# Kernel tuning notes

Hardware: AMD Instinct MI355X
Metric: run time of the kernel (lower is better)

Reference implementation:

```python
import jax, jax.numpy as jnp
import numpy as np

# Gemma-style paged attention, decode-heavy continuous batching
B = 16            # number of sequences in the batch
BLOCK = 64        # KV-cache block size (tokens per block)
MAX_BLOCKS = 32   # max blocks per sequence -> max 2048 KV tokens
NUM_BLOCKS = B * MAX_BLOCKS  # 512 total cache blocks
MAX_KV = MAX_BLOCKS * BLOCK  # 2048
HQ, HK, D = 16, 8, 256       # query heads, kv heads (GQA), head_dim
HIDDEN = 3072
MAX_Q = 4                    # max new (query) tokens per sequence
ROPE_BASE = 10000.0


def setup_inputs() -> dict:
    key = jax.random.key(0)
    ks = jax.random.split(key, 7)
    # deterministic ragged layout
    q_seqlens = np.array([1 + (i % 4) for i in range(B)], np.int64)        # sum = 40
    kv_seqlens = np.array([1024 + (i * 67) % 1025 for i in range(B)], np.int64)
    q_start_loc = np.concatenate([[0], np.cumsum(q_seqlens)[:-1]]).astype(np.int64)
    T = int(q_seqlens.sum())
    history = kv_seqlens - q_seqlens
    position_ids_1d = np.concatenate(
        [np.arange(history[i], kv_seqlens[i]) for i in range(B)]).astype(np.int64)
    block_offsets = np.arange(NUM_BLOCKS, dtype=np.int64).reshape(B, MAX_BLOCKS)
    inv_freq = (1.0 / ROPE_BASE ** (np.arange(0, D, 2) / D)).astype(np.float32)
    return {
        'hidden_states': jax.random.normal(ks[0], (T, HIDDEN), jnp.float32),
        'Wq': jax.random.normal(ks[1], (HIDDEN, HQ * D), jnp.float32) * 0.02,
        'Wk': jax.random.normal(ks[2], (HIDDEN, HK * D), jnp.float32) * 0.02,
        'Wv': jax.random.normal(ks[3], (HIDDEN, HK * D), jnp.float32) * 0.02,
        'Wo': jax.random.normal(ks[4], (HQ * D, HIDDEN), jnp.float32) * 0.02,
        'k_cache': jax.random.normal(ks[5], (NUM_BLOCKS, BLOCK, HK, D), jnp.float32),
        'v_cache': jax.random.normal(ks[6], (NUM_BLOCKS, BLOCK, HK, D), jnp.float32),
        'inv_freq': jnp.asarray(inv_freq),
        'position_ids_1d': jnp.asarray(position_ids_1d),
        'q_start_loc': jnp.asarray(q_start_loc),
        'q_seqlens': jnp.asarray(q_seqlens),
        'kv_seqlens': jnp.asarray(kv_seqlens),
        'block_offsets': jnp.asarray(block_offsets),
    }


def reference(hidden_states, Wq, Wk, Wv, Wo, k_cache, v_cache, inv_freq,
              position_ids_1d, q_start_loc, q_seqlens, kv_seqlens, block_offsets):
    T = hidden_states.shape[0]
    # fused QKV projection
    q = (hidden_states @ Wq).reshape(T, HQ, D)
    k = (hidden_states @ Wk).reshape(T, HK, D)
    v = (hidden_states @ Wv).reshape(T, HK, D)
    # fused rotary embedding (neox / rotate-half style, per-token position ids)
    freqs = position_ids_1d.astype(jnp.float32)[:, None] * inv_freq[None, :]  # [T, D/2]
    cos = jnp.cos(freqs)[:, None, :]
    sin = jnp.sin(freqs)[:, None, :]

    def rope(x):
        x1, x2 = jnp.split(x, 2, axis=-1)
        return jnp.concatenate([x1 * cos - x2 * sin, x2 * cos + x1 * sin], axis=-1)

    q = rope(q)
    k = rope(k)
    # ---- fill_kv_cache: scatter new K/V into paged block cache ----
    tok = jnp.arange(T)
    seq_end = jnp.cumsum(q_seqlens)
    seq_id = jnp.searchsorted(seq_end, tok, side='right')      # sequence of each token
    off = tok - q_start_loc[seq_id]                             # offset within new tokens
    kv_pos = (kv_seqlens - q_seqlens)[seq_id] + off             # absolute kv position
    blk = block_offsets[seq_id, kv_pos // BLOCK]
    slot = kv_pos % BLOCK
    k_cache = k_cache.at[blk, slot].set(k)
    v_cache = v_cache.at[blk, slot].set(v)
    # ---- paged_attention_fwd ----
    # gather each sequence's blocks -> [B, MAX_KV, HK, D]
    k_seq = k_cache[block_offsets].reshape(B, MAX_KV, HK, D)
    v_seq = v_cache[block_offsets].reshape(B, MAX_KV, HK, D)
    # pad queries per sequence -> [B, MAX_Q, HK, G, D]
    qidx = jnp.clip(q_start_loc[:, None] + jnp.arange(MAX_Q)[None, :], 0, T - 1)
    G = HQ // HK
    qpad = q[qidx].reshape(B, MAX_Q, HK, G, D)
    scale = jnp.float32(D) ** -0.5
    scores = jnp.einsum('bqkgd,bskd->bkgqs', qpad * scale, k_seq)  # [B,HK,G,MAX_Q,MAX_KV]
    # causal mask over absolute kv positions (also masks padded kv slots)
    jpos = jnp.arange(MAX_Q)[None, :, None]
    spos = jnp.arange(MAX_KV)[None, None, :]
    mask = spos <= ((kv_seqlens - q_seqlens)[:, None, None] + jpos)  # [B,MAX_Q,MAX_KV]
    scores = jnp.where(mask[:, None, None, :, :], scores, jnp.float32(-1e30))
    attn = jax.nn.softmax(scores, axis=-1)
    out = jnp.einsum('bkgqs,bskd->bqkgd', attn, v_seq).reshape(B, MAX_Q, HQ * D)
    # scatter padded output back to flat token layout
    out_flat = out[seq_id, off]  # [T, HQ*D]
    return out_flat @ Wo
```

## Files before the change

kernel.cpp:

```cpp
#include <hip/hip_runtime.h>
#include <math.h>

#define TT 40
#define NB 16
#define HQn 16
#define HKn 8
#define Gn 2
#define Dn 256
#define HID 3072
#define QKV_COLS 8192
#define NPART 32

#define WAVE_LDS_FENCE() do { \
    asm volatile("s_waitcnt lgkmcnt(0)" ::: "memory"); \
    __builtin_amdgcn_sched_barrier(0); \
  } while (0)

__global__ __launch_bounds__(256) void k1_qkv_gemm(
    const float* __restrict__ hs, const float* __restrict__ Wq,
    const float* __restrict__ Wk, const float* __restrict__ Wv,
    float* __restrict__ part1) {
  const int tile = blockIdx.x & 31;
  const int ks = blockIdx.x >> 5;
  const int c0 = tile << 8;
  const float* W; int ld, cw0;
  if (tile < 16)      { W = Wq; ld = 4096; cw0 = c0; }
  else if (tile < 24) { W = Wk; ld = 2048; cw0 = c0 - 4096; }
  else                { W = Wv; ld = 2048; cw0 = c0 - 6144; }
  const int kbase = ks * 192;
  const int cq = (threadIdx.x & 63) << 2;
  const int r0 = (threadIdx.x >> 6) * 10;
  __shared__ float h_lds[40][64];
  float acc[10][4];
#pragma unroll
  for (int r = 0; r < 10; ++r) { acc[r][0]=0.f; acc[r][1]=0.f; acc[r][2]=0.f; acc[r][3]=0.f; }
  for (int kc = 0; kc < 192; kc += 64) {
    __syncthreads();
    for (int i = threadIdx.x; i < 2560; i += 256) {
      int t = i >> 6, kk = i & 63;
      h_lds[t][kk] = hs[t * HID + kbase + kc + kk];
    }
    __syncthreads();
    const float* wp = W + (size_t)(kbase + kc) * ld + cw0 + cq;
#pragma unroll 2
    for (int k4 = 0; k4 < 16; ++k4) {
      float4 h4[10];
#pragma unroll
      for (int r = 0; r < 10; ++r)
        h4[r] = *reinterpret_cast<const float4*>(&h_lds[r0 + r][k4 << 2]);
#pragma unroll
      for (int j = 0; j < 4; ++j) {
        float4 w4 = *reinterpret_cast<const float4*>(wp + (size_t)((k4 << 2) + j) * ld);
#pragma unroll
        for (int r = 0; r < 10; ++r) {
          float hv = (j == 0) ? h4[r].x : (j == 1) ? h4[r].y
                   : (j == 2) ? h4[r].z : h4[r].w;
          acc[r][0] = fmaf(hv, w4.x, acc[r][0]);
          acc[r][1] = fmaf(hv, w4.y, acc[r][1]);
          acc[r][2] = fmaf(hv, w4.z, acc[r][2]);
          acc[r][3] = fmaf(hv, w4.w, acc[r][3]);
        }
      }
    }
  }
#pragma unroll
  for (int r = 0; r < 10; ++r) {
    int t = r0 + r;
    float4 v = make_float4(acc[r][0], acc[r][1], acc[r][2], acc[r][3]);
    *reinterpret_cast<float4*>(&part1[(size_t)(ks * TT + t) * QKV_COLS + c0 + cq]) = v;
  }
}

__global__ __launch_bounds__(256) void k2_reduce_rope(
    const float* __restrict__ part1, const float* __restrict__ inv_freq,
    const int* __restrict__ pos_ids,
    float* __restrict__ qbuf, float* __restrict__ kbuf, float* __restrict__ vbuf) {
  const int t = blockIdx.x >> 5;
  const int tile = blockIdx.x & 31;
  const int c = (tile << 8) + threadIdx.x;
  float s = 0.f;
#pragma unroll
  for (int ks = 0; ks < 16; ++ks) s += part1[(size_t)(ks * TT + t) * QKV_COLS + c];
  __shared__ float sl[256];
  sl[threadIdx.x] = s;
  __syncthreads();
  if (tile < 24) {
    const int d = threadIdx.x;
    const int d2 = d & 127;
    float fr = (float)pos_ids[t] * inv_freq[d2];
    float cs = cosf(fr), sn = sinf(fr);
    float v = (d < 128) ? (sl[d] * cs - sl[d + 128] * sn)
                        : (sl[d] * cs + sl[d - 128] * sn);
    if (tile < 16) qbuf[t * 4096 + (tile << 8) + d] = v * 0.0625f;
    else           kbuf[t * 2048 + ((tile - 16) << 8) + d] = v;
  } else {
    vbuf[t * 2048 + ((tile - 24) << 8) + threadIdx.x] = s;
  }
}

__global__ __launch_bounds__(256) void k3_attn_partial(
    const float* __restrict__ qbuf, const float* __restrict__ kbuf,
    const float* __restrict__ vbuf, const float* __restrict__ k_cache,
    const float* __restrict__ v_cache, const int* __restrict__ blk_off,
    const int* __restrict__ q_start, const int* __restrict__ q_lens,
    const int* __restrict__ kv_lens,
    float* __restrict__ part_o, float* __restrict__ part_ml) {
  const int seg = blockIdx.x & 7;
  const int hk = (blockIdx.x >> 3) & 7;
  const int b = blockIdx.x >> 6;
  const int kv_len = kv_lens[b];
  if ((seg << 8) >= kv_len) return;
  const int q_cnt = q_lens[b];
  const int hist = kv_len - q_cnt;
  const int q0 = q_start[b];
  const int nq = q_cnt * 2;

  __shared__ float q_lds[8][256];
  __shared__ float S[4][2][64][8];

  const int tid = threadIdx.x;
  const int w = tid >> 6;
  const int lane = tid & 63;

  for (int i = tid; i < 2048; i += 256) {
    int qv = i >> 8, d = i & 255;
    int qtok = min(qv >> 1, q_cnt - 1);
    q_lds[qv][d] = qbuf[(size_t)(q0 + qtok) * 4096 + (hk * Gn + (qv & 1)) * 256 + d];
  }
  __syncthreads();

  const int part = (seg << 2) + w;
  const int sBeg = part << 6;
  if (sBeg >= kv_len) return;

  const int blk = blk_off[(b << 5) + part];
  const float* kb   = k_cache + ((size_t)blk << 17) + ((size_t)hk << 8);
  const float* vb   = v_cache + ((size_t)blk << 17) + ((size_t)hk << 8);
  const float* knew = kbuf + ((size_t)q0 << 11) + ((size_t)hk << 8);
  const float* vnew = vbuf + ((size_t)q0 << 11) + ((size_t)hk << 8);

  const int tp = lane & 7;
  const int qd = lane >> 3;

#pragma unroll
  for (int pass = 0; pass < 2; ++pass) {
    const float* kr[4];
#pragma unroll
    for (int tt = 0; tt < 4; ++tt) {
      int s = sBeg + (pass << 5) + (tp << 2) + tt;
      int sc = s < kv_len ? s : kv_len - 1;
      const float* row = (sc < hist) ? (kb + ((size_t)(sc & 63) << 11))
                                     : (knew + ((size_t)(sc - hist) << 11));
      kr[tt] = row + (qd << 2);
    }
    float acc[4][8];
#pragma unroll
    for (int tt = 0; tt < 4; ++tt)
#pragma unroll
      for (int qv = 0; qv < 8; ++qv) acc[tt][qv] = 0.f;

    float4 kf[2][4];
#pragma unroll
    for (int tt = 0; tt < 4; ++tt)
      kf[0][tt] = *reinterpret_cast<const float4*>(kr[tt]);
#pragma unroll
    for (int c = 0; c < 8; ++c) {
      if (c + 1 < 8) {
#pragma unroll
        for (int tt = 0; tt < 4; ++tt)
          kf[(c + 1) & 1][tt] =
              *reinterpret_cast<const float4*>(kr[tt] + ((c + 1) << 5));
      }
      const float4* kc_ = kf[c & 1];
#pragma unroll
      for (int qv = 0; qv < 8; ++qv) {
        float4 qf = *reinterpret_cast<const float4*>(&q_lds[qv][(qd << 2) + (c << 5)]);
#pragma unroll
        for (int tt = 0; tt < 4; ++tt) {
          acc[tt][qv] = fmaf(qf.x, kc_[tt].x, acc[tt][qv]);
          acc[tt][qv] = fmaf(qf.y, kc_[tt].y, acc[tt][qv]);
          acc[tt][qv] = fmaf(qf.z, kc_[tt].z, acc[tt][qv]);
          acc[tt][qv] = fmaf(qf.w, kc_[tt].w, acc[tt][qv]);
        }
      }
    }
#pragma unroll
    for (int tt = 0; tt < 4; ++tt)
#pragma unroll
      for (int qv = 0; qv < 8; ++qv) {
        float v = acc[tt][qv];
        v += __shfl_xor(v, 8);
        v += __shfl_xor(v, 16);
        acc[tt][qv] = v;
      }
    if ((lane & 24) == 0) {
      const int h = lane >> 5;
#pragma unroll
      for (int tt = 0; tt < 4; ++tt) {
        int srel = (pass << 5) + (tp << 2) + tt;
        *reinterpret_cast<float4*>(&S[w][h][srel][0]) =
            make_float4(acc[tt][0], acc[tt][1], acc[tt][2], acc[tt][3]);
        *reinterpret_cast<float4*>(&S[w][h][srel][4]) =
            make_float4(acc[tt][4], acc[tt][5], acc[tt][6], acc[tt][7]);
      }
    }
  }
  WAVE_LDS_FENCE();

  const int qv2 = lane >> 3;
  const int grp = lane & 7;
  const int pidx8 = (((b * HKn + hk) * NPART + part) << 3);
  float sv[8];
  float mloc = -1e30f;
#pragma unroll
  for (int t = 0; t < 8; ++t) {
    int sl = (t << 3) + grp;
    float v = S[w][0][sl][qv2] + S[w][1][sl][qv2];
    int sAbs = sBeg + sl;
    bool valid = (qv2 < nq) && ((sAbs - hist) <= (qv2 >> 1));
    v = valid ? v : -1e30f;
    sv[t] = v;
    mloc = fmaxf(mloc, v);
  }
  mloc = fmaxf(mloc, __shfl_xor(mloc, 1));
  mloc = fmaxf(mloc, __shfl_xor(mloc, 2));
  mloc = fmaxf(mloc, __shfl_xor(mloc, 4));
  const float M = mloc;
  float lloc = 0.f;
#pragma unroll
  for (int t = 0; t < 8; ++t) {
    float p = __expf(sv[t] - M);
    S[w][0][(t << 3) + grp][qv2] = p;
    lloc += p;
  }
  lloc += __shfl_xor(lloc, 1);
  lloc += __shfl_xor(lloc, 2);
  lloc += __shfl_xor(lloc, 4);
  if (grp == 0)
    *reinterpret_cast<float2*>(&part_ml[(size_t)(pidx8 + qv2) * 2]) =
        make_float2(M, lloc);
  WAVE_LDS_FENCE();

  const int d4 = lane << 2;
  float4 pacc[8];
#pragma unroll
  for (int q = 0; q < 8; ++q) pacc[q] = make_float4(0.f, 0.f, 0.f, 0.f);
  const int lim = min(sBeg + 64, kv_len);

#define PV_STEP(VROW, SREL)                                          \
  {                                                                  \
    float4 vf = *reinterpret_cast<const float4*>(VROW);              \
    float4 p0 = *reinterpret_cast<const float4*>(&S[w][0][SREL][0]); \
    float4 p1 = *reinterpret_cast<const float4*>(&S[w][0][SREL][4]); \
    float pr[8] = {p0.x, p0.y, p0.z, p0.w, p1.x, p1.y, p1.z, p1.w};  \
    _Pragma("unroll")                                                \
    for (int q = 0; q < 8; ++q) {                                    \
      pacc[q].x = fmaf(pr[q], vf.x, pacc[q].x);                      \
      pacc[q].y = fmaf(pr[q], vf.y, pacc[q].y);                      \
      pacc[q].z = fmaf(pr[q], vf.z, pacc[q].z);                      \
      pacc[q].w = fmaf(pr[q], vf.w, pacc[q].w);                      \
    }                                                                \
  }

  {
    int eH = min(lim, hist);
#pragma unroll 4
    for (int s = sBeg; s < eH; ++s)
      PV_STEP(vb + ((size_t)(s & 63) << 11) + d4, s - sBeg);
    int bN = max(sBeg, hist);
    for (int s = bN; s < lim; ++s)
      PV_STEP(vnew + ((size_t)(s - hist) << 11) + d4, s - sBeg);
  }
#undef PV_STEP

#pragma unroll
  for (int q = 0; q < 8; ++q)
    *reinterpret_cast<float4*>(&part_o[(size_t)(pidx8 + q) * 256 + d4]) = pacc[q];
}

__global__ __launch_bounds__(64) void k4_attn_reduce(
    const float* __restrict__ part_o, const float* __restrict__ part_ml,
    const int* __restrict__ q_start, const int* __restrict__ q_lens,
    const int* __restrict__ kv_lens, float* __restrict__ attn_out) {
  const int h = blockIdx.x & 15;
  const int qtok = (blockIdx.x >> 4) & 3;
  const int b = blockIdx.x >> 6;
  const int q_cnt = q_lens[b];
  if (qtok >= q_cnt) return;
  const int kv_len = kv_lens[b];
  const int nparts = (kv_len + 63) >> 6;
  const int qv = qtok * 2 + (h & 1);
  const int hk = h >> 1;
  const int lane = threadIdx.x;
  const int pbase = ((b * HKn + hk) * NPART) << 3;
  float M = -1e30f;
#pragma unroll 4
  for (int i = 0; i < nparts; ++i)
    M = fmaxf(M, part_ml[(size_t)(pbase + (i << 3) + qv) * 2]);
  float4 o = make_float4(0.f, 0.f, 0.f, 0.f);
  float L = 0.f;
#pragma unroll 4
  for (int i = 0; i < nparts; ++i) {
    float2 ml = *reinterpret_cast<const float2*>(
        &part_ml[(size_t)(pbase + (i << 3) + qv) * 2]);
    float corr = __expf(ml.x - M);
    L += corr * ml.y;
    float4 pv = *reinterpret_cast<const float4*>(
        &part_o[(size_t)(pbase + (i << 3) + qv) * 256 + (lane << 2)]);
    o.x = fmaf(corr, pv.x, o.x);
    o.y = fmaf(corr, pv.y, o.y);
    o.z = fmaf(corr, pv.z, o.z);
    o.w = fmaf(corr, pv.w, o.w);
  }
  float inv = 1.0f / L;
  int tr = q_start[b] + qtok;
  float4 res = make_float4(o.x * inv, o.y * inv, o.z * inv, o.w * inv);
  *reinterpret_cast<float4*>(&attn_out[((size_t)tr * HQn + h) * 256 + (lane << 2)]) = res;
}

__global__ __launch_bounds__(256) void k5_out_gemm(
    const float* __restrict__ ain, const float* __restrict__ Wo,
    float* __restrict__ part2) {
  const int tile = blockIdx.x % 12;
  const int ks = blockIdx.x / 12;
  const int c0 = tile << 8;
  const int kbase = ks << 7;
  const int cq = (threadIdx.x & 63) << 2;
  const int r0 = (threadIdx.x >> 6) * 10;
  __shared__ float h_lds[40][64];
  float acc[10][4];
#pragma unroll
  for (int r = 0; r < 10; ++r) { acc[r][0]=0.f; acc[r][1]=0.f; acc[r][2]=0.f; acc[r][3]=0.f; }
  for (int kc = 0; kc < 128; kc += 64) {
    __syncthreads();
    for (int i = threadIdx.x; i < 2560; i += 256) {
      int t = i >> 6, kk = i & 63;
      h_lds[t][kk] = ain[(size_t)t * 4096 + kbase + kc + kk];
    }
    __syncthreads();
    const float* wp = Wo + (size_t)(kbase + kc) * 3072 + c0 + cq;
#pragma unroll 2
    for (int k4 = 0; k4 < 16; ++k4) {
      float4 h4[10];
#pragma unroll
      for (int r = 0; r < 10; ++r)
        h4[r] = *reinterpret_cast<const float4*>(&h_lds[r0 + r][k4 << 2]);
#pragma unroll
      for (int j = 0; j < 4; ++j) {
        float4 w4 = *reinterpret_cast<const float4*>(wp + (size_t)((k4 << 2) + j) * 3072);
#pragma unroll
        for (int r = 0; r < 10; ++r) {
          float hv = (j == 0) ? h4[r].x : (j == 1) ? h4[r].y
                   : (j == 2) ? h4[r].z : h4[r].w;
          acc[r][0] = fmaf(hv, w4.x, acc[r][0]);
          acc[r][1] = fmaf(hv, w4.y, acc[r][1]);
          acc[r][2] = fmaf(hv, w4.z, acc[r][2]);
          acc[r][3] = fmaf(hv, w4.w, acc[r][3]);
        }
      }
    }
  }
#pragma unroll
  for (int r = 0; r < 10; ++r) {
    int t = r0 + r;
    float4 v = make_float4(acc[r][0], acc[r][1], acc[r][2], acc[r][3]);
    *reinterpret_cast<float4*>(&part2[(size_t)(ks * TT + t) * 3072 + c0 + cq]) = v;
  }
}

__global__ __launch_bounds__(256) void k6_final_reduce(
    const float* __restrict__ part2, float* __restrict__ out) {
  const int idx = blockIdx.x * 256 + threadIdx.x;
  float s = 0.f;
#pragma unroll
  for (int ks = 0; ks < 32; ++ks) s += part2[(size_t)ks * 122880 + idx];
  out[idx] = s;
}

extern "C" void kernel_launch(void* const* d_in, const int* in_sizes, int n_in,
                              void* d_out, int out_size, void* d_ws, size_t ws_size,
                              hipStream_t stream) {
  const float* hs       = (const float*)d_in[0];
  const float* Wq       = (const float*)d_in[1];
  const float* Wk       = (const float*)d_in[2];
  const float* Wv       = (const float*)d_in[3];
  const float* Wo       = (const float*)d_in[4];
  const float* k_cache  = (const float*)d_in[5];
  const float* v_cache  = (const float*)d_in[6];
  const float* inv_freq = (const float*)d_in[7];
  const int*   pos_ids  = (const int*)d_in[8];
  const int*   q_start  = (const int*)d_in[9];
  const int*   q_lens   = (const int*)d_in[10];
  const int*   kv_lens  = (const int*)d_in[11];
  const int*   blk_off  = (const int*)d_in[12];

  float* ws = (float*)d_ws;
  float* qbuf     = ws;
  float* kbuf     = ws + 163840;
  float* vbuf     = ws + 245760;
  float* attn_out = ws + 327680;
  float* part1    = ws + 491520;
  float* part_o   = ws + 5734400;
  float* part_ml  = ws + 14123008;
  float* part2    = ws + 14188544;
  float* out      = (float*)d_out;

  k1_qkv_gemm<<<512, 256, 0, stream>>>(hs, Wq, Wk, Wv, part1);
  k2_reduce_rope<<<1280, 256, 0, stream>>>(part1, inv_freq, pos_ids, qbuf, kbuf, vbuf);
  k3_attn_partial<<<1024, 256, 0, stream>>>(qbuf, kbuf, vbuf, k_cache, v_cache,
                                            blk_off, q_start, q_lens, kv_lens,
                                            part_o, part_ml);
  k4_attn_reduce<<<1024, 64, 0, stream>>>(part_o, part_ml, q_start, q_lens,
                                          kv_lens, attn_out);
  k5_out_gemm<<<384, 256, 0, stream>>>(attn_out, Wo, part2);
  k6_final_reduce<<<480, 256, 0, stream>>>(part2, out);
}
```

Measured before the change: 254.3 us.

## Remap attention partial kernel to one block per KV partition covering all KV heads

The attention partial kernel now launches one 512-thread block per (sequence, 64-token partition), with each wave handling one KV head, instead of one block per (sequence, head, 256-token segment) with waves over partitions. The query tile for all heads is loaded once into LDS per block, and the score reduction now spans the full wave through an extra shuffle stage rather than being split across two LDS halves. It also skips writing partial outputs for padded query slots. This changes how K/V cache rows are fetched (each block touches a whole cache block across all heads, which is contiguous) and raises LDS usage and threads per block, which may reduce occupancy.

Measured after the change: 254.7 us. No clear change (+0.2%).

```diff
diff --git a/kernel.cpp b/kernel.cpp
--- a/kernel.cpp
+++ b/kernel.cpp
@@ -98,40 +98,37 @@
   }
 }
 
-__global__ __launch_bounds__(256) void k3_attn_partial(
+__global__ __launch_bounds__(512) void k3_attn_partial(
     const float* __restrict__ qbuf, const float* __restrict__ kbuf,
     const float* __restrict__ vbuf, const float* __restrict__ k_cache,
     const float* __restrict__ v_cache, const int* __restrict__ blk_off,
     const int* __restrict__ q_start, const int* __restrict__ q_lens,
     const int* __restrict__ kv_lens,
     float* __restrict__ part_o, float* __restrict__ part_ml) {
-  const int seg = blockIdx.x & 7;
-  const int hk = (blockIdx.x >> 3) & 7;
-  const int b = blockIdx.x >> 6;
+  const int part = blockIdx.x & 31;
+  const int b = blockIdx.x >> 5;
   const int kv_len = kv_lens[b];
-  if ((seg << 8) >= kv_len) return;
+  const int sBeg = part << 6;
+  if (sBeg >= kv_len) return;
   const int q_cnt = q_lens[b];
   const int hist = kv_len - q_cnt;
   const int q0 = q_start[b];
   const int nq = q_cnt * 2;
 
-  __shared__ float q_lds[8][256];
-  __shared__ float S[4][2][64][8];
+  __shared__ float q_lds[4][16][256];
+  __shared__ float S[8][64][8];
 
   const int tid = threadIdx.x;
-  const int w = tid >> 6;
+  const int hk = tid >> 6;
   const int lane = tid & 63;
 
-  for (int i = tid; i < 2048; i += 256) {
-    int qv = i >> 8, d = i & 255;
-    int qtok = min(qv >> 1, q_cnt - 1);
-    q_lds[qv][d] = qbuf[(size_t)(q0 + qtok) * 4096 + (hk * Gn + (qv & 1)) * 256 + d];
+  const int qtot = q_cnt << 12;
+  for (int i = tid; i < qtot; i += 512) {
+    int qtok = i >> 12;
+    int rem = i & 4095;
+    q_lds[qtok][rem >> 8][rem & 255] = qbuf[(size_t)(q0 + qtok) * 4096 + rem];
   }
   __syncthreads();
-
-  const int part = (seg << 2) + w;
-  const int sBeg = part << 6;
-  if (sBeg >= kv_len) return;
 
   const int blk = blk_off[(b << 5) + part];
   const float* kb   = k_cache + ((size_t)blk << 17) + ((size_t)hk << 8);
@@ -141,6 +138,7 @@
 
   const int tp = lane & 7;
   const int qd = lane >> 3;
+  const int qc1 = q_cnt - 1;
 
 #pragma unroll
   for (int pass = 0; pass < 2; ++pass) {
@@ -174,7 +172,10 @@
       const float4* kc_ = kf[c & 1];
 #pragma unroll
       for (int qv = 0; qv < 8; ++qv) {
-        float4 qf = *reinterpret_cast<const float4*>(&q_lds[qv][(qd << 2) + (c << 5)]);
+        int qtok = min(qv >> 1, qc1);
+        int head = (hk << 1) + (qv & 1);
+        float4 qf = *reinterpret_cast<const float4*>(
+            &q_lds[qtok][head][(qd << 2) + (c << 5)]);
 #pragma unroll
         for (int tt = 0; tt < 4; ++tt) {
           acc[tt][qv] = fmaf(qf.x, kc_[tt].x, acc[tt][qv]);
@@ -191,16 +192,16 @@
         float v = acc[tt][qv];
         v += __shfl_xor(v, 8);
         v += __shfl_xor(v, 16);
+        v += __shfl_xor(v, 32);
         acc[tt][qv] = v;
       }
-    if ((lane & 24) == 0) {
-      const int h = lane >> 5;
+    if (lane < 8) {
 #pragma unroll
       for (int tt = 0; tt < 4; ++tt) {
         int srel = (pass << 5) + (tp << 2) + tt;
-        *reinterpret_cast<float4*>(&S[w][h][srel][0]) =
+        *reinterpret_cast<float4*>(&S[hk][srel][0]) =
             make_float4(acc[tt][0], acc[tt][1], acc[tt][2], acc[tt][3]);
-        *reinterpret_cast<float4*>(&S[w][h][srel][4]) =
+        *reinterpret_cast<float4*>(&S[hk][srel][4]) =
             make_float4(acc[tt][4], acc[tt][5], acc[tt][6], acc[tt][7]);
       }
     }
@@ -215,7 +216,7 @@
 #pragma unroll
   for (int t = 0; t < 8; ++t) {
     int sl = (t << 3) + grp;
-    float v = S[w][0][sl][qv2] + S[w][1][sl][qv2];
+    float v = S[hk][sl][qv2];
     int sAbs = sBeg + sl;
     bool valid = (qv2 < nq) && ((sAbs - hist) <= (qv2 >> 1));
     v = valid ? v : -1e30f;
@@ -230,7 +231,7 @@
 #pragma unroll
   for (int t = 0; t < 8; ++t) {
     float p = __expf(sv[t] - M);
-    S[w][0][(t << 3) + grp][qv2] = p;
+    S[hk][(t << 3) + grp][qv2] = p;
     lloc += p;
   }
   lloc += __shfl_xor(lloc, 1);
@@ -250,8 +251,8 @@
 #define PV_STEP(VROW, SREL)                                          \
   {                                                                  \
     float4 vf = *reinterpret_cast<const float4*>(VROW);              \
-    float4 p0 = *reinterpret_cast<const float4*>(&S[w][0][SREL][0]); \
-    float4 p1 = *reinterpret_cast<const float4*>(&S[w][0][SREL][4]); \
+    float4 p0 = *reinterpret_cast<const float4*>(&S[hk][SREL][0]);   \
+    float4 p1 = *reinterpret_cast<const float4*>(&S[hk][SREL][4]);   \
     float pr[8] = {p0.x, p0.y, p0.z, p0.w, p1.x, p1.y, p1.z, p1.w};  \
     _Pragma("unroll")                                                \
     for (int q = 0; q < 8; ++q) {                                    \
@@ -275,7 +276,8 @@
 
 #pragma unroll
   for (int q = 0; q < 8; ++q)
-    *reinterpret_cast<float4*>(&part_o[(size_t)(pidx8 + q) * 256 + d4]) = pacc[q];
+    if (q < nq)
+      *reinterpret_cast<float4*>(&part_o[(size_t)(pidx8 + q) * 256 + d4]) = pacc[q];
 }
 
 __global__ __launch_bounds__(64) void k4_attn_reduce(
@@ -407,9 +409,9 @@
 
   k1_qkv_gemm<<<512, 256, 0, stream>>>(hs, Wq, Wk, Wv, part1);
   k2_reduce_rope<<<1280, 256, 0, stream>>>(part1, inv_freq, pos_ids, qbuf, kbuf, vbuf);
-  k3_attn_partial<<<1024, 256, 0, stream>>>(qbuf, kbuf, vbuf, k_cache, v_cache,
-                                            blk_off, q_start, q_lens, kv_lens,
-                                            part_o, part_ml);
+  k3_attn_partial<<<512, 512, 0, stream>>>(qbuf, kbuf, vbuf, k_cache, v_cache,
+                                           blk_off, q_start, q_lens, kv_lens,
+                                           part_o, part_ml);
   k4_attn_reduce<<<1024, 64, 0, stream>>>(part_o, part_ml, q_start, q_lens,
                                           kv_lens, attn_out);
   k5_out_gemm<<<384, 256, 0, stream>>>(attn_out, Wo, part2);
```
